# Kernel tuning notes

Hardware: AMD Instinct MI355X
Metric: run time of the kernel (lower is better)

Reference implementation:

```python
import jax, jax.numpy as jnp
import numpy as np

D_MODEL, D_INNER, D_STATE, D_CONV, DT_RANK = 512, 1024, 16, 4, 32
B, L = 2, 2048
EPS = 1e-5


def setup_inputs() -> dict:
    key = jax.random.key(0)
    ks = jax.random.split(key, 10)
    s = 0.02
    return {
        "x": jax.random.normal(ks[0], (B, L, D_MODEL), jnp.float32),
        "attention_mask": jnp.ones((B, L), jnp.int32),
        "norm_weight": jnp.ones((D_MODEL,), jnp.float32),
        "in_proj_w": jax.random.normal(ks[1], (2 * D_INNER, D_MODEL), jnp.float32) * s,
        "conv_w": jax.random.normal(ks[2], (D_INNER, 1, D_CONV), jnp.float32) * 0.3,
        "conv_b": jnp.zeros((D_INNER,), jnp.float32),
        "x_proj_w": jax.random.normal(ks[3], (DT_RANK + 2 * D_STATE, D_INNER), jnp.float32) * s,
        "dt_proj_w": jax.random.normal(ks[4], (D_INNER, DT_RANK), jnp.float32) * 0.1,
        "dt_proj_b": jnp.full((D_INNER,), -4.6, jnp.float32),  # softplus ~ 0.01
        "A_log": jnp.log(jnp.tile(jnp.arange(1, D_STATE + 1, dtype=jnp.float32), (D_INNER, 1))),
        "D": jnp.ones((D_INNER,), jnp.float32),
        "out_proj_w": jax.random.normal(ks[5], (D_MODEL, D_INNER), jnp.float32) * s,
    }


def _mamba_block(h, in_proj_w, conv_w, conv_b, x_proj_w, dt_proj_w, dt_proj_b, A_log, D, out_proj_w):
    # in_proj -> split into x, z  (B, L, D_INNER) each
    xz = jnp.einsum("bld,ed->ble", h, in_proj_w)
    u, z = jnp.split(xz, 2, axis=-1)
    # causal depthwise conv over time, then SiLU
    u_ncl = jnp.transpose(u, (0, 2, 1))  # (B, D_INNER, L)
    conv = jax.lax.conv_general_dilated(
        u_ncl, conv_w, window_strides=(1,), padding=[(D_CONV - 1, 0)],
        feature_group_count=D_INNER, dimension_numbers=("NCH", "OIH", "NCH"))
    u = jax.nn.silu(jnp.transpose(conv + conv_b[None, :, None], (0, 2, 1)))  # (B, L, D_INNER)
    # x_proj -> dt (low rank), Bm, Cm
    xdbc = jnp.einsum("bld,ed->ble", u, x_proj_w)
    dt_r, Bm, Cm = jnp.split(xdbc, [DT_RANK, DT_RANK + D_STATE], axis=-1)
    dt = jax.nn.softplus(jnp.einsum("blr,dr->bld", dt_r, dt_proj_w) + dt_proj_b)  # (B,L,D_INNER)
    A = -jnp.exp(A_log)  # (D_INNER, D_STATE)

    def step(hstate, inputs):
        dt_t, B_t, C_t, u_t = inputs  # (B,Din), (B,Dst), (B,Dst), (B,Din)
        dA = jnp.exp(dt_t[..., None] * A)                      # (B, Din, Dst)
        dBu = dt_t[..., None] * B_t[:, None, :] * u_t[..., None]
        hstate = dA * hstate + dBu
        y_t = jnp.einsum("bds,bs->bd", hstate, C_t)
        return hstate, y_t

    xs = (jnp.swapaxes(dt, 0, 1), jnp.swapaxes(Bm, 0, 1), jnp.swapaxes(Cm, 0, 1), jnp.swapaxes(u, 0, 1))
    h0 = jnp.zeros((u.shape[0], D_INNER, D_STATE), u.dtype)
    _, ys = jax.lax.scan(step, h0, xs)
    y = jnp.swapaxes(ys, 0, 1) + D * u          # skip term
    y = y * jax.nn.silu(z)                      # gating
    return jnp.einsum("ble,de->bld", y, out_proj_w)


def reference(x, attention_mask, norm_weight, in_proj_w, conv_w, conv_b,
              x_proj_w, dt_proj_w, dt_proj_b, A_log, D, out_proj_w):
    # pre-norm RMSNorm
    var = jnp.mean(jnp.square(x), axis=-1, keepdims=True)
    h = x * jax.lax.rsqrt(var + EPS) * norm_weight
    mask = attention_mask[..., None].astype(h.dtype)
    h = h * mask
    h = _mamba_block(h, in_proj_w, conv_w, conv_b, x_proj_w, dt_proj_w, dt_proj_b, A_log, D, out_proj_w)
    h = h * mask
    return x + h
```

## Files before the change

### kernel.cpp

```cpp
#include <hip/hip_runtime.h>
#include <hip/hip_bf16.h>
#include <math.h>

#define D_MODEL 512
#define D_INNER 1024
#define D_STATE 16
#define DT_RANK 32
#define B_SZ 2
#define SEQ 2048
#define ROWS (B_SZ*SEQ)
#define EPSV 1e-5f
#define NCHUNK 64
#define CLEN (SEQ/NCHUNK)
#define NPAIR (B_SZ*D_INNER)
#define LOG2E 1.44269504088896f
#define N_ALL 1088

typedef short bf16x8 __attribute__((ext_vector_type(8)));
typedef float f32x4  __attribute__((ext_vector_type(4)));
typedef __hip_bfloat16 bf16_t;

static __device__ __forceinline__ float bf2f(bf16_t v) { return __bfloat162float(v); }

__global__ __launch_bounds__(256) void convert_bf16_kernel(const float* __restrict__ in,
        bf16_t* __restrict__ out, int n4) {
    int i = blockIdx.x * 256 + threadIdx.x;
    if (i >= n4) return;
    float4 v = reinterpret_cast<const float4*>(in)[i];
    bf16_t o[4] = {__float2bfloat16(v.x), __float2bfloat16(v.y),
                   __float2bfloat16(v.z), __float2bfloat16(v.w)};
    reinterpret_cast<ushort4*>(out)[i] = *reinterpret_cast<ushort4*>(o);
}

__global__ __launch_bounds__(256) void wc_gemm(const float* __restrict__ dt_proj_w,
        const float* __restrict__ x_proj_w, bf16_t* __restrict__ W_all) {
    __shared__ float a[64][33];
    __shared__ float b[32][68];
    int tid = threadIdx.x;
    int n0 = (blockIdx.x >> 4) * 64;
    int k0 = (blockIdx.x & 15) * 64;
    #pragma unroll
    for (int h = 0; h < 2; ++h) {
        int q = tid + h * 256;
        int r = q >> 3, c = (q & 7) * 4;
        float4 v = *reinterpret_cast<const float4*>(dt_proj_w + (size_t)(n0 + r) * DT_RANK + c);
        a[r][c] = v.x; a[r][c + 1] = v.y; a[r][c + 2] = v.z; a[r][c + 3] = v.w;
        int r2 = q >> 4, c2 = (q & 15) * 4;
        float4 w = *reinterpret_cast<const float4*>(x_proj_w + (size_t)r2 * D_INNER + k0 + c2);
        b[r2][c2] = w.x; b[r2][c2 + 1] = w.y; b[r2][c2 + 2] = w.z; b[r2][c2 + 3] = w.w;
    }
    __syncthreads();
    int ty = tid >> 4, tx = tid & 15;
    float acc[4][4] = {};
    #pragma unroll
    for (int r = 0; r < 32; ++r) {
        float av[4], bv[4];
        #pragma unroll
        for (int i = 0; i < 4; ++i) av[i] = a[ty * 4 + i][r];
        #pragma unroll
        for (int j = 0; j < 4; ++j) bv[j] = b[r][tx * 4 + j];
        #pragma unroll
        for (int i = 0; i < 4; ++i)
            #pragma unroll
            for (int j = 0; j < 4; ++j)
                acc[i][j] = fmaf(av[i], bv[j], acc[i][j]);
    }
    #pragma unroll
    for (int i = 0; i < 4; ++i) {
        bf16_t o[4];
        #pragma unroll
        for (int j = 0; j < 4; ++j) o[j] = __float2bfloat16(acc[i][j]);
        *reinterpret_cast<ushort4*>(W_all + (size_t)(n0 + ty * 4 + i) * D_INNER + k0 + tx * 4) =
            *reinterpret_cast<ushort4*>(o);
    }
}

__global__ __launch_bounds__(256) void wall_tail(const float* __restrict__ x_proj_w,
        bf16_t* __restrict__ W_all) {
    int idx = blockIdx.x * 256 + threadIdx.x;
    int row = idx >> 8, cq = (idx & 255) * 4;
    bf16_t o[4] = {};
    if (row < 32) {
        float4 v = *reinterpret_cast<const float4*>(x_proj_w + (size_t)(32 + row) * D_INNER + cq);
        o[0] = __float2bfloat16(v.x); o[1] = __float2bfloat16(v.y);
        o[2] = __float2bfloat16(v.z); o[3] = __float2bfloat16(v.w);
    }
    *reinterpret_cast<ushort4*>(W_all + (size_t)(1024 + row) * D_INNER + cq) =
        *reinterpret_cast<ushort4*>(o);
}

__global__ __launch_bounds__(256) void rmsnorm_kernel(const float* __restrict__ x,
        const int* __restrict__ mask, const float* __restrict__ w, bf16_t* __restrict__ h) {
    int row = blockIdx.x;
    int tid = threadIdx.x;
    const float2 v = reinterpret_cast<const float2*>(x + (size_t)row * D_MODEL)[tid];
    float ss = v.x * v.x + v.y * v.y;
    #pragma unroll
    for (int m = 1; m < 64; m <<= 1) ss += __shfl_xor(ss, m);
    __shared__ float red[4];
    if ((tid & 63) == 0) red[tid >> 6] = ss;
    __syncthreads();
    float tot = red[0] + red[1] + red[2] + red[3];
    float scale = rsqrtf(tot * (1.0f / D_MODEL) + EPSV) * (float)mask[row];
    __hip_bfloat162 o;
    o.x = __float2bfloat16(v.x * scale * w[2 * tid]);
    o.y = __float2bfloat16(v.y * scale * w[2 * tid + 1]);
    reinterpret_cast<__hip_bfloat162*>(h + (size_t)row * D_MODEL)[tid] = o;
}

template<int MODE>
__global__ __launch_bounds__(256) void gemm_mfma(
        const bf16_t* __restrict__ A, const bf16_t* __restrict__ Bw,
        void* __restrict__ Cv, int M, int N, int K,
        const float* __restrict__ xres, const int* __restrict__ mask2,
        void* __restrict__ z2, const float* __restrict__ bias) {
    __shared__ alignas(16) bf16_t As[64 * 64];
    __shared__ alignas(16) bf16_t Bs[64 * 64];
    const int tid = threadIdx.x;
    const int wid = tid >> 6, lane = tid & 63;
    const int m0 = blockIdx.y * 64, n0 = blockIdx.x * 64;
    const int wr = (wid >> 1) * 32, wc = (wid & 1) * 32;

    f32x4 acc[2][2];
    #pragma unroll
    for (int i = 0; i < 2; ++i)
        #pragma unroll
        for (int j = 0; j < 2; ++j)
            #pragma unroll
            for (int r = 0; r < 4; ++r) acc[i][j][r] = 0.f;

    const int rrow = lane & 15, kg = lane >> 4;
    const int lrow = lane >> 3;
    const int cbs = (lane & 7) ^ lrow;

    for (int k0 = 0; k0 < K; k0 += 64) {
        #pragma unroll
        for (int j = 0; j < 2; ++j) {
            int c = wid * 2 + j;
            int r = c * 8 + lrow;
            const bf16_t* ga = A  + (size_t)(m0 + r) * K + k0 + cbs * 8;
            const bf16_t* gb = Bw + (size_t)(n0 + r) * K + k0 + cbs * 8;
            __builtin_amdgcn_global_load_lds(
                (const __attribute__((address_space(1))) void*)ga,
                (__attribute__((address_space(3))) void*)(As + c * 512), 16, 0, 0);
            __builtin_amdgcn_global_load_lds(
                (const __attribute__((address_space(1))) void*)gb,
                (__attribute__((address_space(3))) void*)(Bs + c * 512), 16, 0, 0);
        }
        __syncthreads();

        #pragma unroll
        for (int kk = 0; kk < 2; ++kk) {
            bf16x8 af[2], bfr[2];
            int g = kk * 4 + kg;
            #pragma unroll
            for (int i = 0; i < 2; ++i) {
                int ra = wr + i * 16 + rrow;
                af[i] = *reinterpret_cast<const bf16x8*>(As + ra * 64 + ((g ^ (ra & 7)) * 8));
                int rb = wc + i * 16 + rrow;
                bfr[i] = *reinterpret_cast<const bf16x8*>(Bs + rb * 64 + ((g ^ (rb & 7)) * 8));
            }
            #pragma unroll
            for (int i = 0; i < 2; ++i)
                #pragma unroll
                for (int j = 0; j < 2; ++j)
                    acc[i][j] = __builtin_amdgcn_mfma_f32_16x16x32_bf16(af[i], bfr[j], acc[i][j], 0, 0, 0);
        }
        __syncthreads();
    }

    #pragma unroll
    for (int i = 0; i < 2; ++i)
        #pragma unroll
        for (int j = 0; j < 2; ++j)
            #pragma unroll
            for (int rg = 0; rg < 4; ++rg) {
                int m = m0 + wr + i * 16 + (lane >> 4) * 4 + rg;
                int n = n0 + wc + j * 16 + (lane & 15);
                float v = acc[i][j][rg];
                if (MODE == 2) {
                    ((float*)Cv)[(size_t)m * N + n] = xres[(size_t)m * N + n] + (float)mask2[m] * v;
                } else if (MODE == 3) {
                    if (n < D_INNER)
                        ((bf16_t*)Cv)[(size_t)m * D_INNER + n] = __float2bfloat16(v);
                    else
                        ((bf16_t*)z2)[(size_t)m * D_INNER + (n - D_INNER)] = __float2bfloat16(v);
                } else {
                    if (n < D_INNER) {
                        float s = v + bias[n];
                        s = (s > 20.f) ? s : log1pf(expf(s));
                        ((bf16_t*)Cv)[(size_t)m * D_INNER + n] = __float2bfloat16(s);
                    } else if (n < D_INNER + 32) {
                        ((float*)z2)[(size_t)m * 32 + (n - D_INNER)] = v;
                    }
                }
            }
}

__global__ __launch_bounds__(256) void conv_silu_kernel(const bf16_t* __restrict__ upre,
        const float* __restrict__ conv_w, const float* __restrict__ conv_b,
        bf16_t* __restrict__ u) {
    int idx = blockIdx.x * 256 + threadIdx.x;
    int dp = idx & 511;
    int row = idx >> 9;
    int t = row & (SEQ - 1);
    const __hip_bfloat162* base =
        reinterpret_cast<const __hip_bfloat162*>(upre + (size_t)(row - t) * D_INNER) + dp;
    int d0 = 2 * dp;
    float sx = conv_b[d0], sy = conv_b[d0 + 1];
    #pragma unroll
    for (int j = 0; j < 4; ++j) {
        int tt = t - 3 + j;
        if (tt >= 0) {
            __hip_bfloat162 vv = base[(size_t)tt * 512];
            sx = fmaf(conv_w[d0 * 4 + j], bf2f(vv.x), sx);
            sy = fmaf(conv_w[(d0 + 1) * 4 + j], bf2f(vv.y), sy);
        }
    }
    __hip_bfloat162 o;
    o.x = __float2bfloat16(sx / (1.f + __expf(-sx)));
    o.y = __float2bfloat16(sy / (1.f + __expf(-sy)));
    reinterpret_cast<__hip_bfloat162*>(u)[idx] = o;
}

__global__ __launch_bounds__(256) void scan_phase1(
        const bf16_t* __restrict__ dtb, const bf16_t* __restrict__ ub,
        const float* __restrict__ bcbuf, const float* __restrict__ A_log,
        float* __restrict__ P, float* __restrict__ F) {
    int tid = threadIdx.x;
    int bid = blockIdx.x;
    int dblk = bid & 3, c = (bid >> 2) & (NCHUNK - 1), b = bid >> 8;
    int d = dblk * 256 + tid;
    __shared__ float sBC[CLEN][32];
    size_t rb = (size_t)b * SEQ + (size_t)c * CLEN;
    {
        int row = tid >> 3, q = tid & 7;
        *reinterpret_cast<float4*>(&sBC[row][q * 4]) =
            *reinterpret_cast<const float4*>(bcbuf + (rb + row) * 32 + q * 4);
    }
    float A2[16];
    #pragma unroll
    for (int s4 = 0; s4 < 4; ++s4) {
        float4 a = *reinterpret_cast<const float4*>(A_log + d * D_STATE + s4 * 4);
        A2[s4 * 4 + 0] = -expf(a.x) * LOG2E;
        A2[s4 * 4 + 1] = -expf(a.y) * LOG2E;
        A2[s4 * 4 + 2] = -expf(a.z) * LOG2E;
        A2[s4 * 4 + 3] = -expf(a.w) * LOG2E;
    }
    float p[16], f[16];
    #pragma unroll
    for (int s = 0; s < 16; ++s) { p[s] = 1.f; f[s] = 0.f; }
    const bf16_t* dtp = dtb + rb * D_INNER + d;
    const bf16_t* up  = ub  + rb * D_INNER + d;
    __syncthreads();
    float dtv = bf2f(dtp[0]), uv = bf2f(up[0]);
    for (int t = 0; t < CLEN; ++t) {
        int tn = (t + 1 < CLEN) ? t + 1 : t;
        float dt_n = bf2f(dtp[(size_t)tn * D_INNER]);
        float u_n  = bf2f(up[(size_t)tn * D_INNER]);
        float dtu = dtv * uv;
        #pragma unroll
        for (int s = 0; s < 16; ++s) {
            float e = exp2f(dtv * A2[s]);
            p[s] *= e;
            f[s] = fmaf(e, f[s], sBC[t][s] * dtu);
        }
        dtv = dt_n; uv = u_n;
    }
    size_t o = ((size_t)(b * D_INNER + d) * NCHUNK + c) * D_STATE;
    #pragma unroll
    for (int s4 = 0; s4 < 4; ++s4) {
        float4 vp = {p[s4*4+0], p[s4*4+1], p[s4*4+2], p[s4*4+3]};
        float4 vf = {f[s4*4+0], f[s4*4+1], f[s4*4+2], f[s4*4+3]};
        *reinterpret_cast<float4*>(P + o + s4 * 4) = vp;
        *reinterpret_cast<float4*>(F + o + s4 * 4) = vf;
    }
}

__global__ __launch_bounds__(256) void scan_phase2(
        float* __restrict__ P, const float* __restrict__ F) {
    int idx = blockIdx.x * 256 + threadIdx.x;
    int pair = idx >> 4, s = idx & 15;
    size_t base = (size_t)pair * NCHUNK * D_STATE + s;
    float h = 0.f;
    for (int c = 0; c < NCHUNK; ++c) {
        size_t o = base + (size_t)c * D_STATE;
        float pp = P[o], ff = F[o];
        P[o] = h;
        h = fmaf(pp, h, ff);
    }
}

__global__ __launch_bounds__(256) void scan_phase3(
        const bf16_t* __restrict__ dtb, const bf16_t* __restrict__ ub,
        const float* __restrict__ bcbuf, const bf16_t* __restrict__ zbuf,
        const float* __restrict__ A_log, const float* __restrict__ Dw,
        const float* __restrict__ Hinit, bf16_t* __restrict__ ybuf) {
    int tid = threadIdx.x;
    int bid = blockIdx.x;
    int dblk = bid & 3, c = (bid >> 2) & (NCHUNK - 1), b = bid >> 8;
    int d = dblk * 256 + tid;
    __shared__ float sBC[CLEN][32];
    size_t rb = (size_t)b * SEQ + (size_t)c * CLEN;
    {
        int row = tid >> 3, q = tid & 7;
        *reinterpret_cast<float4*>(&sBC[row][q * 4]) =
            *reinterpret_cast<const float4*>(bcbuf + (rb + row) * 32 + q * 4);
    }
    float A2[16];
    #pragma unroll
    for (int s4 = 0; s4 < 4; ++s4) {
        float4 a = *reinterpret_cast<const float4*>(A_log + d * D_STATE + s4 * 4);
        A2[s4 * 4 + 0] = -expf(a.x) * LOG2E;
        A2[s4 * 4 + 1] = -expf(a.y) * LOG2E;
        A2[s4 * 4 + 2] = -expf(a.z) * LOG2E;
        A2[s4 * 4 + 3] = -expf(a.w) * LOG2E;
    }
    float Dd = Dw[d];
    float st[16];
    size_t o = ((size_t)(b * D_INNER + d) * NCHUNK + c) * D_STATE;
    #pragma unroll
    for (int s4 = 0; s4 < 4; ++s4) {
        float4 hv = *reinterpret_cast<const float4*>(Hinit + o + s4 * 4);
        st[s4*4+0] = hv.x; st[s4*4+1] = hv.y; st[s4*4+2] = hv.z; st[s4*4+3] = hv.w;
    }
    const bf16_t* dtp = dtb + rb * D_INNER + d;
    const bf16_t* up  = ub  + rb * D_INNER + d;
    const bf16_t* zp  = zbuf + rb * D_INNER + d;
    bf16_t* yp = ybuf + rb * D_INNER + d;
    __syncthreads();
    float dtv = bf2f(dtp[0]), uv = bf2f(up[0]), zv = bf2f(zp[0]);
    for (int t = 0; t < CLEN; ++t) {
        int tn = (t + 1 < CLEN) ? t + 1 : t;
        float dt_n = bf2f(dtp[(size_t)tn * D_INNER]);
        float u_n  = bf2f(up[(size_t)tn * D_INNER]);
        float z_n  = bf2f(zp[(size_t)tn * D_INNER]);
        float dtu = dtv * uv;
        float y = 0.f;
        #pragma unroll
        for (int s = 0; s < 16; ++s) {
            float e = exp2f(dtv * A2[s]);
            st[s] = fmaf(e, st[s], sBC[t][s] * dtu);
            y = fmaf(st[s], sBC[t][16 + s], y);
        }
        float sig = 1.f / (1.f + __expf(-zv));
        yp[(size_t)t * D_INNER] = __float2bfloat16((y + Dd * uv) * (zv * sig));
        dtv = dt_n; uv = u_n; zv = z_n;
    }
}

extern "C" void kernel_launch(void* const* d_in, const int* in_sizes, int n_in,
                              void* d_out, int out_size, void* d_ws, size_t ws_size,
                              hipStream_t stream) {
    const float* x          = (const float*)d_in[0];
    const int*   mask       = (const int*)d_in[1];
    const float* norm_w     = (const float*)d_in[2];
    const float* in_proj_w  = (const float*)d_in[3];
    const float* conv_w     = (const float*)d_in[4];
    const float* conv_b     = (const float*)d_in[5];
    const float* x_proj_w   = (const float*)d_in[6];
    const float* dt_proj_w  = (const float*)d_in[7];
    const float* dt_proj_b  = (const float*)d_in[8];
    const float* A_log      = (const float*)d_in[9];
    const float* Dw         = (const float*)d_in[10];
    const float* out_proj_w = (const float*)d_in[11];
    float* out = (float*)d_out;
    float* ws  = (float*)d_ws;

    bf16_t* u_pre = (bf16_t*)ws;
    bf16_t* zbuf  = (bf16_t*)(ws + 2097152);
    bf16_t* u_bf  = (bf16_t*)(ws + 6291456);
    bf16_t* dt_bf = (bf16_t*)(ws + 8388608);
    bf16_t* h_bf  = (bf16_t*)(ws + 10485760);
    bf16_t* y_bf  = (bf16_t*)(ws + 10485760);
    float*  bcbuf = ws + 12582912;
    float*  Pbuf  = ws + 12845056;
    bf16_t* w_in  = (bf16_t*)(ws + 12845056);
    float*  Fbuf  = ws + 14942208;
    bf16_t* W_all = (bf16_t*)(ws + 14942208);
    bf16_t* w_out = (bf16_t*)(ws + 17039360);

    convert_bf16_kernel<<<1024, 256, 0, stream>>>(in_proj_w, w_in, 2 * D_INNER * D_MODEL / 4);
    convert_bf16_kernel<<<512, 256, 0, stream>>>(out_proj_w, w_out, D_MODEL * D_INNER / 4);
    wc_gemm<<<256, 256, 0, stream>>>(dt_proj_w, x_proj_w, W_all);
    wall_tail<<<64, 256, 0, stream>>>(x_proj_w, W_all);
    rmsnorm_kernel<<<ROWS, 256, 0, stream>>>(x, mask, norm_w, h_bf);
    gemm_mfma<3><<<dim3(32, 64), 256, 0, stream>>>(
        h_bf, w_in, u_pre, ROWS, 2 * D_INNER, D_MODEL, nullptr, nullptr, zbuf, nullptr);
    conv_silu_kernel<<<(ROWS * D_INNER / 2) / 256, 256, 0, stream>>>(u_pre, conv_w, conv_b, u_bf);
    gemm_mfma<4><<<dim3(N_ALL / 64, 64), 256, 0, stream>>>(
        u_bf, W_all, dt_bf, ROWS, N_ALL, D_INNER, nullptr, nullptr, bcbuf, dt_proj_b);
    scan_phase1<<<B_SZ * NCHUNK * 4, 256, 0, stream>>>(dt_bf, u_bf, bcbuf, A_log, Pbuf, Fbuf);
    scan_phase2<<<NPAIR * D_STATE / 256, 256, 0, stream>>>(Pbuf, Fbuf);
    scan_phase3<<<B_SZ * NCHUNK * 4, 256, 0, stream>>>(dt_bf, u_bf, bcbuf, zbuf, A_log, Dw,
                                                       Pbuf, y_bf);
    gemm_mfma<2><<<dim3(8, 64), 256, 0, stream>>>(
        y_bf, w_out, out, ROWS, D_MODEL, D_INNER, x, mask, nullptr, nullptr);
}
```

Before: 186.5 us.

## Merge prep kernels, add XCD swizzle to GEMMs, prefetch-unroll scan loops

Five setup launches (two weight converts, the dt/x-proj weight product, its tail, and RMSNorm) are folded into one prep kernel that dispatches on block index, cutting launch overhead and serialization. The MFMA GEMMs remap block indices so neighbouring tiles land on the same XCD for better L2 reuse. Scan phases 1 and 3 now prefetch dt/u/z four timesteps ahead in register batches, and phase 2 prefetches eight chunks ahead, to hide global-load latency. The costs are more register pressure and a large heterogeneous kernel whose branches use different amounts of shared memory.

Result: faster. 180.2 us (-3.3%).

```diff
diff --git a/kernel.cpp b/kernel.cpp
--- a/kernel.cpp
+++ b/kernel.cpp
@@ -22,90 +22,99 @@
 
 static __device__ __forceinline__ float bf2f(bf16_t v) { return __bfloat162float(v); }
 
-__global__ __launch_bounds__(256) void convert_bf16_kernel(const float* __restrict__ in,
-        bf16_t* __restrict__ out, int n4) {
-    int i = blockIdx.x * 256 + threadIdx.x;
-    if (i >= n4) return;
-    float4 v = reinterpret_cast<const float4*>(in)[i];
-    bf16_t o[4] = {__float2bfloat16(v.x), __float2bfloat16(v.y),
-                   __float2bfloat16(v.z), __float2bfloat16(v.w)};
-    reinterpret_cast<ushort4*>(out)[i] = *reinterpret_cast<ushort4*>(o);
-}
-
-__global__ __launch_bounds__(256) void wc_gemm(const float* __restrict__ dt_proj_w,
-        const float* __restrict__ x_proj_w, bf16_t* __restrict__ W_all) {
-    __shared__ float a[64][33];
-    __shared__ float b[32][68];
+static __device__ __forceinline__ void xcd_swizzle(int& bx, int& by) {
+    int gx = gridDim.x;
+    int nwg = gx * gridDim.y;
+    int flat = by * gx + bx;
+    int q = nwg >> 3;
+    int s = (flat & 7) * q + (flat >> 3);
+    bx = s % gx; by = s / gx;
+}
+
+__global__ __launch_bounds__(256) void prep_kernel(
+        const float* __restrict__ in_proj_w, const float* __restrict__ out_proj_w,
+        const float* __restrict__ dt_proj_w, const float* __restrict__ x_proj_w,
+        const float* __restrict__ x, const int* __restrict__ mask,
+        const float* __restrict__ norm_w,
+        bf16_t* __restrict__ w_in, bf16_t* __restrict__ w_out,
+        bf16_t* __restrict__ W_all, bf16_t* __restrict__ h) {
+    int bid = blockIdx.x;
     int tid = threadIdx.x;
-    int n0 = (blockIdx.x >> 4) * 64;
-    int k0 = (blockIdx.x & 15) * 64;
-    #pragma unroll
-    for (int h = 0; h < 2; ++h) {
-        int q = tid + h * 256;
-        int r = q >> 3, c = (q & 7) * 4;
-        float4 v = *reinterpret_cast<const float4*>(dt_proj_w + (size_t)(n0 + r) * DT_RANK + c);
-        a[r][c] = v.x; a[r][c + 1] = v.y; a[r][c + 2] = v.z; a[r][c + 3] = v.w;
-        int r2 = q >> 4, c2 = (q & 15) * 4;
-        float4 w = *reinterpret_cast<const float4*>(x_proj_w + (size_t)r2 * D_INNER + k0 + c2);
-        b[r2][c2] = w.x; b[r2][c2 + 1] = w.y; b[r2][c2 + 2] = w.z; b[r2][c2 + 3] = w.w;
-    }
-    __syncthreads();
-    int ty = tid >> 4, tx = tid & 15;
-    float acc[4][4] = {};
-    #pragma unroll
-    for (int r = 0; r < 32; ++r) {
-        float av[4], bv[4];
-        #pragma unroll
-        for (int i = 0; i < 4; ++i) av[i] = a[ty * 4 + i][r];
-        #pragma unroll
-        for (int j = 0; j < 4; ++j) bv[j] = b[r][tx * 4 + j];
-        #pragma unroll
-        for (int i = 0; i < 4; ++i)
-            #pragma unroll
-            for (int j = 0; j < 4; ++j)
-                acc[i][j] = fmaf(av[i], bv[j], acc[i][j]);
-    }
-    #pragma unroll
-    for (int i = 0; i < 4; ++i) {
-        bf16_t o[4];
-        #pragma unroll
-        for (int j = 0; j < 4; ++j) o[j] = __float2bfloat16(acc[i][j]);
-        *reinterpret_cast<ushort4*>(W_all + (size_t)(n0 + ty * 4 + i) * D_INNER + k0 + tx * 4) =
+    if (bid < 1536) {
+        const float* src = (bid < 1024) ? in_proj_w : out_proj_w;
+        bf16_t* dst = (bid < 1024) ? w_in : w_out;
+        int i = ((bid < 1024) ? bid : (bid - 1024)) * 256 + tid;
+        float4 v = reinterpret_cast<const float4*>(src)[i];
+        bf16_t o[4] = {__float2bfloat16(v.x), __float2bfloat16(v.y),
+                       __float2bfloat16(v.z), __float2bfloat16(v.w)};
+        reinterpret_cast<ushort4*>(dst)[i] = *reinterpret_cast<ushort4*>(o);
+    } else if (bid < 1792) {
+        __shared__ float a[64][33];
+        __shared__ float b[32][68];
+        int blk = bid - 1536;
+        int n0 = (blk >> 4) * 64;
+        int k0 = (blk & 15) * 64;
+        #pragma unroll
+        for (int hh = 0; hh < 2; ++hh) {
+            int q = tid + hh * 256;
+            int r = q >> 3, c = (q & 7) * 4;
+            float4 v = *reinterpret_cast<const float4*>(dt_proj_w + (size_t)(n0 + r) * DT_RANK + c);
+            a[r][c] = v.x; a[r][c + 1] = v.y; a[r][c + 2] = v.z; a[r][c + 3] = v.w;
+            int r2 = q >> 4, c2 = (q & 15) * 4;
+            float4 w = *reinterpret_cast<const float4*>(x_proj_w + (size_t)r2 * D_INNER + k0 + c2);
+            b[r2][c2] = w.x; b[r2][c2 + 1] = w.y; b[r2][c2 + 2] = w.z; b[r2][c2 + 3] = w.w;
+        }
+        __syncthreads();
+        int ty = tid >> 4, tx = tid & 15;
+        float acc[4][4] = {};
+        #pragma unroll
+        for (int r = 0; r < 32; ++r) {
+            float av[4], bv[4];
+            #pragma unroll
+            for (int i = 0; i < 4; ++i) av[i] = a[ty * 4 + i][r];
+            #pragma unroll
+            for (int j = 0; j < 4; ++j) bv[j] = b[r][tx * 4 + j];
+            #pragma unroll
+            for (int i = 0; i < 4; ++i)
+                #pragma unroll
+                for (int j = 0; j < 4; ++j)
+                    acc[i][j] = fmaf(av[i], bv[j], acc[i][j]);
+        }
+        #pragma unroll
+        for (int i = 0; i < 4; ++i) {
+            bf16_t o[4];
+            #pragma unroll
+            for (int j = 0; j < 4; ++j) o[j] = __float2bfloat16(acc[i][j]);
+            *reinterpret_cast<ushort4*>(W_all + (size_t)(n0 + ty * 4 + i) * D_INNER + k0 + tx * 4) =
+                *reinterpret_cast<ushort4*>(o);
+        }
+    } else if (bid < 1856) {
+        int idx = (bid - 1792) * 256 + tid;
+        int row = idx >> 8, cq = (idx & 255) * 4;
+        bf16_t o[4] = {};
+        if (row < 32) {
+            float4 v = *reinterpret_cast<const float4*>(x_proj_w + (size_t)(32 + row) * D_INNER + cq);
+            o[0] = __float2bfloat16(v.x); o[1] = __float2bfloat16(v.y);
+            o[2] = __float2bfloat16(v.z); o[3] = __float2bfloat16(v.w);
+        }
+        *reinterpret_cast<ushort4*>(W_all + (size_t)(1024 + row) * D_INNER + cq) =
             *reinterpret_cast<ushort4*>(o);
-    }
-}
-
-__global__ __launch_bounds__(256) void wall_tail(const float* __restrict__ x_proj_w,
-        bf16_t* __restrict__ W_all) {
-    int idx = blockIdx.x * 256 + threadIdx.x;
-    int row = idx >> 8, cq = (idx & 255) * 4;
-    bf16_t o[4] = {};
-    if (row < 32) {
-        float4 v = *reinterpret_cast<const float4*>(x_proj_w + (size_t)(32 + row) * D_INNER + cq);
-        o[0] = __float2bfloat16(v.x); o[1] = __float2bfloat16(v.y);
-        o[2] = __float2bfloat16(v.z); o[3] = __float2bfloat16(v.w);
-    }
-    *reinterpret_cast<ushort4*>(W_all + (size_t)(1024 + row) * D_INNER + cq) =
-        *reinterpret_cast<ushort4*>(o);
-}
-
-__global__ __launch_bounds__(256) void rmsnorm_kernel(const float* __restrict__ x,
-        const int* __restrict__ mask, const float* __restrict__ w, bf16_t* __restrict__ h) {
-    int row = blockIdx.x;
-    int tid = threadIdx.x;
-    const float2 v = reinterpret_cast<const float2*>(x + (size_t)row * D_MODEL)[tid];
-    float ss = v.x * v.x + v.y * v.y;
-    #pragma unroll
-    for (int m = 1; m < 64; m <<= 1) ss += __shfl_xor(ss, m);
-    __shared__ float red[4];
-    if ((tid & 63) == 0) red[tid >> 6] = ss;
-    __syncthreads();
-    float tot = red[0] + red[1] + red[2] + red[3];
-    float scale = rsqrtf(tot * (1.0f / D_MODEL) + EPSV) * (float)mask[row];
-    __hip_bfloat162 o;
-    o.x = __float2bfloat16(v.x * scale * w[2 * tid]);
-    o.y = __float2bfloat16(v.y * scale * w[2 * tid + 1]);
-    reinterpret_cast<__hip_bfloat162*>(h + (size_t)row * D_MODEL)[tid] = o;
+    } else {
+        __shared__ float red[4];
+        int row = bid - 1856;
+        const float2 v = reinterpret_cast<const float2*>(x + (size_t)row * D_MODEL)[tid];
+        float ss = v.x * v.x + v.y * v.y;
+        #pragma unroll
+        for (int m = 1; m < 64; m <<= 1) ss += __shfl_xor(ss, m);
+        if ((tid & 63) == 0) red[tid >> 6] = ss;
+        __syncthreads();
+        float tot = red[0] + red[1] + red[2] + red[3];
+        float scale = rsqrtf(tot * (1.0f / D_MODEL) + EPSV) * (float)mask[row];
+        __hip_bfloat162 o;
+        o.x = __float2bfloat16(v.x * scale * norm_w[2 * tid]);
+        o.y = __float2bfloat16(v.y * scale * norm_w[2 * tid + 1]);
+        reinterpret_cast<__hip_bfloat162*>(h + (size_t)row * D_MODEL)[tid] = o;
+    }
 }
 
 template<int MODE>
@@ -118,7 +127,9 @@
     __shared__ alignas(16) bf16_t Bs[64 * 64];
     const int tid = threadIdx.x;
     const int wid = tid >> 6, lane = tid & 63;
-    const int m0 = blockIdx.y * 64, n0 = blockIdx.x * 64;
+    int bx = blockIdx.x, by = blockIdx.y;
+    xcd_swizzle(bx, by);
+    const int m0 = by * 64, n0 = bx * 64;
     const int wr = (wid >> 1) * 32, wc = (wid & 1) * 32;
 
     f32x4 acc[2][2];
@@ -252,20 +263,38 @@
     for (int s = 0; s < 16; ++s) { p[s] = 1.f; f[s] = 0.f; }
     const bf16_t* dtp = dtb + rb * D_INNER + d;
     const bf16_t* up  = ub  + rb * D_INNER + d;
+    float dtc[4], uc[4];
+    #pragma unroll
+    for (int j = 0; j < 4; ++j) {
+        dtc[j] = bf2f(dtp[(size_t)j * D_INNER]);
+        uc[j]  = bf2f(up[(size_t)j * D_INNER]);
+    }
     __syncthreads();
-    float dtv = bf2f(dtp[0]), uv = bf2f(up[0]);
-    for (int t = 0; t < CLEN; ++t) {
-        int tn = (t + 1 < CLEN) ? t + 1 : t;
-        float dt_n = bf2f(dtp[(size_t)tn * D_INNER]);
-        float u_n  = bf2f(up[(size_t)tn * D_INNER]);
-        float dtu = dtv * uv;
-        #pragma unroll
-        for (int s = 0; s < 16; ++s) {
-            float e = exp2f(dtv * A2[s]);
-            p[s] *= e;
-            f[s] = fmaf(e, f[s], sBC[t][s] * dtu);
-        }
-        dtv = dt_n; uv = u_n;
+    for (int tb = 0; tb < CLEN; tb += 4) {
+        float dtn[4], un[4];
+        if (tb + 4 < CLEN) {
+            #pragma unroll
+            for (int j = 0; j < 4; ++j) {
+                dtn[j] = bf2f(dtp[(size_t)(tb + 4 + j) * D_INNER]);
+                un[j]  = bf2f(up[(size_t)(tb + 4 + j) * D_INNER]);
+            }
+        } else {
+            #pragma unroll
+            for (int j = 0; j < 4; ++j) { dtn[j] = 0.f; un[j] = 0.f; }
+        }
+        #pragma unroll
+        for (int j = 0; j < 4; ++j) {
+            float dtv = dtc[j];
+            float dtu = dtv * uc[j];
+            #pragma unroll
+            for (int s = 0; s < 16; ++s) {
+                float e = exp2f(dtv * A2[s]);
+                p[s] *= e;
+                f[s] = fmaf(e, f[s], sBC[tb + j][s] * dtu);
+            }
+        }
+        #pragma unroll
+        for (int j = 0; j < 4; ++j) { dtc[j] = dtn[j]; uc[j] = un[j]; }
     }
     size_t o = ((size_t)(b * D_INNER + d) * NCHUNK + c) * D_STATE;
     #pragma unroll
@@ -282,12 +311,26 @@
     int idx = blockIdx.x * 256 + threadIdx.x;
     int pair = idx >> 4, s = idx & 15;
     size_t base = (size_t)pair * NCHUNK * D_STATE + s;
+    float pp[8], ff[8];
+    #pragma unroll
+    for (int j = 0; j < 8; ++j) {
+        pp[j] = P[base + (size_t)j * D_STATE];
+        ff[j] = F[base + (size_t)j * D_STATE];
+    }
     float h = 0.f;
-    for (int c = 0; c < NCHUNK; ++c) {
-        size_t o = base + (size_t)c * D_STATE;
-        float pp = P[o], ff = F[o];
-        P[o] = h;
-        h = fmaf(pp, h, ff);
+    #pragma unroll
+    for (int cb = 0; cb < 8; ++cb) {
+        #pragma unroll
+        for (int j = 0; j < 8; ++j) {
+            int c = cb * 8 + j;
+            float p = pp[j], f = ff[j];
+            if (cb < 7) {
+                pp[j] = P[base + (size_t)(c + 8) * D_STATE];
+                ff[j] = F[base + (size_t)(c + 8) * D_STATE];
+            }
+            P[base + (size_t)c * D_STATE] = h;
+            h = fmaf(p, h, f);
+        }
     }
 }
 
@@ -328,24 +371,44 @@
     const bf16_t* up  = ub  + rb * D_INNER + d;
     const bf16_t* zp  = zbuf + rb * D_INNER + d;
     bf16_t* yp = ybuf + rb * D_INNER + d;
+    float dtc[4], uc[4], zc[4];
+    #pragma unroll
+    for (int j = 0; j < 4; ++j) {
+        dtc[j] = bf2f(dtp[(size_t)j * D_INNER]);
+        uc[j]  = bf2f(up[(size_t)j * D_INNER]);
+        zc[j]  = bf2f(zp[(size_t)j * D_INNER]);
+    }
     __syncthreads();
-    float dtv = bf2f(dtp[0]), uv = bf2f(up[0]), zv = bf2f(zp[0]);
-    for (int t = 0; t < CLEN; ++t) {
-        int tn = (t + 1 < CLEN) ? t + 1 : t;
-        float dt_n = bf2f(dtp[(size_t)tn * D_INNER]);
-        float u_n  = bf2f(up[(size_t)tn * D_INNER]);
-        float z_n  = bf2f(zp[(size_t)tn * D_INNER]);
-        float dtu = dtv * uv;
-        float y = 0.f;
-        #pragma unroll
-        for (int s = 0; s < 16; ++s) {
-            float e = exp2f(dtv * A2[s]);
-            st[s] = fmaf(e, st[s], sBC[t][s] * dtu);
-            y = fmaf(st[s], sBC[t][16 + s], y);
-        }
-        float sig = 1.f / (1.f + __expf(-zv));
-        yp[(size_t)t * D_INNER] = __float2bfloat16((y + Dd * uv) * (zv * sig));
-        dtv = dt_n; uv = u_n; zv = z_n;
+    for (int tb = 0; tb < CLEN; tb += 4) {
+        float dtn[4], un[4], zn[4];
+        if (tb + 4 < CLEN) {
+            #pragma unroll
+            for (int j = 0; j < 4; ++j) {
+                dtn[j] = bf2f(dtp[(size_t)(tb + 4 + j) * D_INNER]);
+                un[j]  = bf2f(up[(size_t)(tb + 4 + j) * D_INNER]);
+                zn[j]  = bf2f(zp[(size_t)(tb + 4 + j) * D_INNER]);
+            }
+        } else {
+            #pragma unroll
+            for (int j = 0; j < 4; ++j) { dtn[j] = 0.f; un[j] = 0.f; zn[j] = 0.f; }
+        }
+        #pragma unroll
+        for (int j = 0; j < 4; ++j) {
+            float dtv = dtc[j];
+            float dtu = dtv * uc[j];
+            float y = 0.f;
+            #pragma unroll
+            for (int s = 0; s < 16; ++s) {
+                float e = exp2f(dtv * A2[s]);
+                st[s] = fmaf(e, st[s], sBC[tb + j][s] * dtu);
+                y = fmaf(st[s], sBC[tb + j][16 + s], y);
+            }
+            float zv = zc[j];
+            float sig = 1.f / (1.f + __expf(-zv));
+            yp[(size_t)(tb + j) * D_INNER] = __float2bfloat16((y + Dd * uc[j]) * (zv * sig));
+        }
+        #pragma unroll
+        for (int j = 0; j < 4; ++j) { dtc[j] = dtn[j]; uc[j] = un[j]; zc[j] = zn[j]; }
     }
 }
 
@@ -380,11 +443,8 @@
     bf16_t* W_all = (bf16_t*)(ws + 14942208);
     bf16_t* w_out = (bf16_t*)(ws + 17039360);
 
-    convert_bf16_kernel<<<1024, 256, 0, stream>>>(in_proj_w, w_in, 2 * D_INNER * D_MODEL / 4);
-    convert_bf16_kernel<<<512, 256, 0, stream>>>(out_proj_w, w_out, D_MODEL * D_INNER / 4);
-    wc_gemm<<<256, 256, 0, stream>>>(dt_proj_w, x_proj_w, W_all);
-    wall_tail<<<64, 256, 0, stream>>>(x_proj_w, W_all);
-    rmsnorm_kernel<<<ROWS, 256, 0, stream>>>(x, mask, norm_w, h_bf);
+    prep_kernel<<<5952, 256, 0, stream>>>(in_proj_w, out_proj_w, dt_proj_w, x_proj_w,
+                                          x, mask, norm_w, w_in, w_out, W_all, h_bf);
     gemm_mfma<3><<<dim3(32, 64), 256, 0, stream>>>(
         h_bf, w_in, u_pre, ROWS, 2 * D_INNER, D_MODEL, nullptr, nullptr, zbuf, nullptr);
     conv_silu_kernel<<<(ROWS * D_INNER / 2) / 256, 256, 0, stream>>>(u_pre, conv_w, conv_b, u_bf);
```
